# Kernel optimization log

Measured on AMD Instinct MI355X. Metric: run time of the kernel, lower is better.

The kernel has to match this reference:

```python
import jax, jax.numpy as jnp
import numpy as np

TEMPERATURE = 8.0  # sqrt(d_k), d_k = 64

def setup_inputs() -> dict:
    key = jax.random.key(0)
    k1, k2, k3, k4 = jax.random.split(key, 4)
    B, H, S, D = 2, 16, 2048, 64
    q = jax.random.normal(k1, (B, H, S, D), dtype=jnp.float32)
    k = jax.random.normal(k2, (B, H, S, D), dtype=jnp.float32)
    v = jax.random.normal(k3, (B, H, S, D), dtype=jnp.float32)
    # dwm: distance-weight matrix broadcast over heads
    dwm = jax.random.uniform(k4, (B, 1, S, S), dtype=jnp.float32)
    sigma = jnp.ones((1,), dtype=jnp.float32)
    return {"q": q, "k": k, "v": v, "dwm": dwm, "sigma": sigma}

def reference(q, k, v, dwm, sigma):
    # scores: [B,H,S,S]
    attn = jnp.einsum("bhsd,bhtd->bhst", q / TEMPERATURE, k)
    g = jnp.exp(dwm / (sigma ** 2))  # broadcasts [B,1,S,S] -> [B,H,S,S]
    attn = jnp.abs(attn * g)
    attn = jax.nn.softmax(attn, axis=-1)  # dropout is identity in eval
    output = jnp.einsum("bhst,bhtd->bhsd", attn, v)
    return (output, attn)
```

## Files before the change

### kernel.cpp

```cpp
#include <hip/hip_runtime.h>
#include <hip/hip_fp16.h>

#define NB 2
#define NH 16
#define NS 2048
#define ND 64
#define BM 64
#define BN 64
#define KP 72
#define VP 72
#define PP 72

typedef _Float16 half8 __attribute__((ext_vector_type(8)));
typedef float f32x4 __attribute__((ext_vector_type(4)));

__global__ __launch_bounds__(256, 4)
void attn_fused(const float* __restrict__ qg, const float* __restrict__ kgl,
                const float* __restrict__ vgl, const float* __restrict__ dwm,
                const float* __restrict__ sig, float* __restrict__ out0,
                float* __restrict__ attn)
{
    __shared__ _Float16 Khi[BN * KP];
    __shared__ _Float16 Klo[BN * KP];
    __shared__ _Float16 Vs[ND * VP];
    __shared__ _Float16 Ps[BM * PP];

    const int tid  = threadIdx.x;
    const int wave = tid >> 6;
    const int lane = tid & 63;
    const int quad = lane >> 4;
    const int lc   = lane & 15;

    const int mtile = blockIdx.x;
    const int bh    = blockIdx.y;
    const int b     = bh >> 4;

    const float sv = sig[0];
    const float inv_s2 = 1.0f / (sv * sv);

    const float* qp = qg  + (size_t)bh * NS * ND + (size_t)mtile * BM * ND;
    const float* kp = kgl + (size_t)bh * NS * ND;
    const float* vp = vgl + (size_t)bh * NS * ND;
    const float* dp = dwm + (size_t)b  * NS * NS + (size_t)mtile * BM * NS;
    float* op = out0 + (size_t)bh * NS * ND + (size_t)mtile * BM * ND;
    float* ap = attn + (size_t)bh * NS * NS + (size_t)mtile * BM * NS;

    half8 aqh0, aql0, aqh1, aql1;
    {
        const float* qr = qp + (size_t)(wave * 16 + lc) * ND + quad * 8;
        float4 f0 = *(const float4*)qr;
        float4 f1 = *(const float4*)(qr + 4);
        float4 f2 = *(const float4*)(qr + 32);
        float4 f3 = *(const float4*)(qr + 36);
        float v0[8] = {f0.x, f0.y, f0.z, f0.w, f1.x, f1.y, f1.z, f1.w};
        float v1[8] = {f2.x, f2.y, f2.z, f2.w, f3.x, f3.y, f3.z, f3.w};
        #pragma unroll
        for (int j = 0; j < 8; j++) {
            float x = v0[j] * 0.125f;
            _Float16 h = (_Float16)x;
            aqh0[j] = h; aql0[j] = (_Float16)(x - (float)h);
            x = v1[j] * 0.125f;
            h = (_Float16)x;
            aqh1[j] = h; aql1[j] = (_Float16)(x - (float)h);
        }
    }

    auto stageK = [&](int t0) {
        const int r  = tid >> 2;
        const int ds = (tid & 3) * 16;
        const float* s = kp + (size_t)(t0 + r) * ND + ds;
        float4 f0 = *(const float4*)s;
        float4 f1 = *(const float4*)(s + 4);
        float4 f2 = *(const float4*)(s + 8);
        float4 f3 = *(const float4*)(s + 12);
        float fv[16] = {f0.x, f0.y, f0.z, f0.w, f1.x, f1.y, f1.z, f1.w,
                        f2.x, f2.y, f2.z, f2.w, f3.x, f3.y, f3.z, f3.w};
        half8 h0, h1, l0, l1;
        #pragma unroll
        for (int i = 0; i < 8; i++) {
            _Float16 h = (_Float16)fv[i];
            h0[i] = h; l0[i] = (_Float16)(fv[i] - (float)h);
            h = (_Float16)fv[8 + i];
            h1[i] = h; l1[i] = (_Float16)(fv[8 + i] - (float)h);
        }
        *(half8*)&Khi[r * KP + ds]     = h0;
        *(half8*)&Khi[r * KP + ds + 8] = h1;
        *(half8*)&Klo[r * KP + ds]     = l0;
        *(half8*)&Klo[r * KP + ds + 8] = l1;
    };

    auto stageV = [&](int t0) {
        const int tp = tid >> 3;
        const int ds = (tid & 7) * 8;
        const float4* sa = (const float4*)(vp + (size_t)(t0 + 2 * tp) * ND + ds);
        const float4* sb = (const float4*)(vp + (size_t)(t0 + 2 * tp + 1) * ND + ds);
        float4 a0 = sa[0], a1 = sa[1];
        float4 b0 = sb[0], b1 = sb[1];
        float av[8] = {a0.x, a0.y, a0.z, a0.w, a1.x, a1.y, a1.z, a1.w};
        float bv[8] = {b0.x, b0.y, b0.z, b0.w, b1.x, b1.y, b1.z, b1.w};
        unsigned int* Vdw = (unsigned int*)Vs;
        #pragma unroll
        for (int i = 0; i < 8; i++) {
            const int d  = ds + i;
            const int dw = d * (VP / 2) + (tp ^ (((d >> 3) & 7) << 2));
            union { _Float16 h[2]; unsigned int u; } pk;
            pk.h[0] = (_Float16)av[i];
            pk.h[1] = (_Float16)bv[i];
            Vdw[dw] = pk.u;
        }
    };

    float lsum[4] = {0.f, 0.f, 0.f, 0.f};

    for (int t0 = 0; t0 < NS; t0 += BN) {
        __syncthreads();
        stageK(t0);
        __syncthreads();
        #pragma unroll
        for (int n = 0; n < 4; n++) {
            const half8 kh0 = *(const half8*)&Khi[(n * 16 + lc) * KP + quad * 8];
            const half8 kh1 = *(const half8*)&Khi[(n * 16 + lc) * KP + quad * 8 + 32];
            const half8 kl0 = *(const half8*)&Klo[(n * 16 + lc) * KP + quad * 8];
            const half8 kl1 = *(const half8*)&Klo[(n * 16 + lc) * KP + quad * 8 + 32];
            f32x4 c = {0.f, 0.f, 0.f, 0.f};
            c = __builtin_amdgcn_mfma_f32_16x16x32_f16(aqh0, kh0, c, 0, 0, 0);
            c = __builtin_amdgcn_mfma_f32_16x16x32_f16(aqh1, kh1, c, 0, 0, 0);
            c = __builtin_amdgcn_mfma_f32_16x16x32_f16(aql0, kh0, c, 0, 0, 0);
            c = __builtin_amdgcn_mfma_f32_16x16x32_f16(aql1, kh1, c, 0, 0, 0);
            c = __builtin_amdgcn_mfma_f32_16x16x32_f16(aqh0, kl0, c, 0, 0, 0);
            c = __builtin_amdgcn_mfma_f32_16x16x32_f16(aqh1, kl1, c, 0, 0, 0);
            #pragma unroll
            for (int r2 = 0; r2 < 4; r2++) {
                const int lrow = wave * 16 + quad * 4 + r2;
                const int col  = t0 + n * 16 + lc;
                const float g = __expf(dp[(size_t)lrow * NS + col] * inv_s2);
                const float z = fabsf(c[r2] * g);
                lsum[r2] += __expf(z);
            }
        }
    }

    #pragma unroll
    for (int r2 = 0; r2 < 4; r2++) {
        float s = lsum[r2];
        s += __shfl_xor(s, 1, 64);
        s += __shfl_xor(s, 2, 64);
        s += __shfl_xor(s, 4, 64);
        s += __shfl_xor(s, 8, 64);
        lsum[r2] = 1.0f / s;
    }

    f32x4 o[4];
    #pragma unroll
    for (int i = 0; i < 4; i++) o[i] = (f32x4){0.f, 0.f, 0.f, 0.f};

    for (int t0 = 0; t0 < NS; t0 += BN) {
        __syncthreads();
        stageK(t0);
        stageV(t0);
        __syncthreads();
        #pragma unroll
        for (int n = 0; n < 4; n++) {
            const half8 kh0 = *(const half8*)&Khi[(n * 16 + lc) * KP + quad * 8];
            const half8 kh1 = *(const half8*)&Khi[(n * 16 + lc) * KP + quad * 8 + 32];
            const half8 kl0 = *(const half8*)&Klo[(n * 16 + lc) * KP + quad * 8];
            const half8 kl1 = *(const half8*)&Klo[(n * 16 + lc) * KP + quad * 8 + 32];
            f32x4 c = {0.f, 0.f, 0.f, 0.f};
            c = __builtin_amdgcn_mfma_f32_16x16x32_f16(aqh0, kh0, c, 0, 0, 0);
            c = __builtin_amdgcn_mfma_f32_16x16x32_f16(aqh1, kh1, c, 0, 0, 0);
            c = __builtin_amdgcn_mfma_f32_16x16x32_f16(aql0, kh0, c, 0, 0, 0);
            c = __builtin_amdgcn_mfma_f32_16x16x32_f16(aql1, kh1, c, 0, 0, 0);
            c = __builtin_amdgcn_mfma_f32_16x16x32_f16(aqh0, kl0, c, 0, 0, 0);
            c = __builtin_amdgcn_mfma_f32_16x16x32_f16(aqh1, kl1, c, 0, 0, 0);
            #pragma unroll
            for (int r2 = 0; r2 < 4; r2++) {
                const int lrow = wave * 16 + quad * 4 + r2;
                const int col  = t0 + n * 16 + lc;
                const float g = __expf(dp[(size_t)lrow * NS + col] * inv_s2);
                const float z = fabsf(c[r2] * g);
                const float p = __expf(z) * lsum[r2];
                Ps[(size_t)lrow * PP + n * 16 + lc] = (_Float16)p;
            }
        }
        const half8 pa0 = *(const half8*)&Ps[(wave * 16 + lc) * PP + quad * 8];
        const half8 pa1 = *(const half8*)&Ps[(wave * 16 + lc) * PP + quad * 8 + 32];

        {
            float* arow = ap + (size_t)(wave * 16 + lc) * NS + t0 + quad * 8;
            f32x4 s0 = {(float)pa0[0], (float)pa0[1], (float)pa0[2], (float)pa0[3]};
            f32x4 s1 = {(float)pa0[4], (float)pa0[5], (float)pa0[6], (float)pa0[7]};
            f32x4 s2 = {(float)pa1[0], (float)pa1[1], (float)pa1[2], (float)pa1[3]};
            f32x4 s3 = {(float)pa1[4], (float)pa1[5], (float)pa1[6], (float)pa1[7]};
            __builtin_nontemporal_store(s0, (f32x4*)arow);
            __builtin_nontemporal_store(s1, (f32x4*)(arow + 4));
            __builtin_nontemporal_store(s2, (f32x4*)(arow + 32));
            __builtin_nontemporal_store(s3, (f32x4*)(arow + 36));
        }

        #pragma unroll
        for (int n2 = 0; n2 < 4; n2++) {
            const int dv  = n2 * 16 + lc;
            const int fd  = ((dv >> 3) & 7) << 2;
            const int dwb = dv * (VP / 2);
            const half8 bv0 = *(const half8*)((const char*)Vs +
                               (size_t)((dwb + ((quad * 4) ^ fd)) * 4));
            const half8 bv1 = *(const half8*)((const char*)Vs +
                               (size_t)((dwb + ((16 + quad * 4) ^ fd)) * 4));
            o[n2] = __builtin_amdgcn_mfma_f32_16x16x32_f16(pa0, bv0, o[n2], 0, 0, 0);
            o[n2] = __builtin_amdgcn_mfma_f32_16x16x32_f16(pa1, bv1, o[n2], 0, 0, 0);
        }
    }

    #pragma unroll
    for (int n2 = 0; n2 < 4; n2++) {
        #pragma unroll
        for (int r2 = 0; r2 < 4; r2++) {
            const int lrow = wave * 16 + quad * 4 + r2;
            __builtin_nontemporal_store(o[n2][r2],
                                        &op[(size_t)lrow * ND + n2 * 16 + lc]);
        }
    }
}

extern "C" void kernel_launch(void* const* d_in, const int* in_sizes, int n_in,
                              void* d_out, int out_size, void* d_ws, size_t ws_size,
                              hipStream_t stream) {
    (void)in_sizes; (void)n_in; (void)out_size; (void)d_ws; (void)ws_size;
    const float* q   = (const float*)d_in[0];
    const float* k   = (const float*)d_in[1];
    const float* v   = (const float*)d_in[2];
    const float* dwm = (const float*)d_in[3];
    const float* sig = (const float*)d_in[4];
    float* out0 = (float*)d_out;
    float* attn = out0 + (size_t)NB * NH * NS * ND;
    dim3 grid(NS / BM, NB * NH);
    attn_fused<<<grid, dim3(256), 0, stream>>>(q, k, v, dwm, sig, out0, attn);
}
```

Baseline: 810.6 us.

## Pre-convert K/V to swizzled fp16 tiles and stream them via global_load_lds

Adds a prep kernel that splits K into hi/lo fp16 and transposes V into fp16, writing XOR-swizzled tile images to the workspace. The main kernel copies these images straight into LDS with global_load_lds. This removes the per-workgroup fp32 load, conversion and transpose work that was repeated for every query tile. It also remaps workgroup IDs so blocks sharing a head run close together, and raises the occupancy hint to 5 blocks per CU. The costs are an extra kernel launch, a workspace round trip, and a fallback path that only runs when the workspace is too small.

```diff
diff --git a/kernel.cpp b/kernel.cpp
--- a/kernel.cpp
+++ b/kernel.cpp
@@ -7,23 +7,266 @@
 #define ND 64
 #define BM 64
 #define BN 64
+#define NT (NS / BN)
+#define TILE_BYTES 24576
+#define KV_BYTES ((size_t)NB * NH * NT * TILE_BYTES)
+
+#define SW(r) ((((r) & 7) ^ (((r) & 8) >> 2)) << 4)
+
+typedef _Float16 half8 __attribute__((ext_vector_type(8)));
+typedef _Float16 half4 __attribute__((ext_vector_type(4)));
+typedef float f32x4 __attribute__((ext_vector_type(4)));
+
+#define GLDS16(gp, lp) __builtin_amdgcn_global_load_lds(                      \
+    (const __attribute__((address_space(1))) void*)(gp),                      \
+    (__attribute__((address_space(3))) void*)(lp), 16, 0, 0)
+
+__global__ __launch_bounds__(256)
+void prep_kv(const float* __restrict__ kg, const float* __restrict__ vg,
+             char* __restrict__ ws)
+{
+    __shared__ _Float16 T[64][72];
+    const int tile = blockIdx.x, bh = blockIdx.y, tid = threadIdx.x;
+    const float* kp = kg + ((size_t)bh * NS + (size_t)tile * BN) * ND;
+    const float* vp = vg + ((size_t)bh * NS + (size_t)tile * BN) * ND;
+    char* img = ws + ((size_t)(bh * NT + tile)) * TILE_BYTES;
+
+    #pragma unroll
+    for (int i = 0; i < 2; ++i) {
+        const int c = tid + i * 256;
+        const int r = c >> 3, s = c & 7;
+        const float* src = kp + r * ND + s * 8;
+        float4 f0 = *(const float4*)src;
+        float4 f1 = *(const float4*)(src + 4);
+        float fv[8] = {f0.x, f0.y, f0.z, f0.w, f1.x, f1.y, f1.z, f1.w};
+        half8 h, l;
+        #pragma unroll
+        for (int j = 0; j < 8; ++j) {
+            _Float16 hh = (_Float16)fv[j];
+            h[j] = hh; l[j] = (_Float16)(fv[j] - (float)hh);
+        }
+        const int off = r * 128 + ((s << 4) ^ SW(r));
+        *(half8*)(img + off) = h;
+        *(half8*)(img + 8192 + off) = l;
+    }
+    #pragma unroll
+    for (int i = 0; i < 2; ++i) {
+        const int c = tid + i * 256;
+        const int t = c >> 3, ds = (c & 7) * 8;
+        const float* src = vp + t * ND + ds;
+        float4 f0 = *(const float4*)src;
+        float4 f1 = *(const float4*)(src + 4);
+        float fv[8] = {f0.x, f0.y, f0.z, f0.w, f1.x, f1.y, f1.z, f1.w};
+        #pragma unroll
+        for (int j = 0; j < 8; ++j) T[t][ds + j] = (_Float16)fv[j];
+    }
+    __syncthreads();
+    #pragma unroll
+    for (int i = 0; i < 2; ++i) {
+        const int c = tid + i * 256;
+        const int d = c >> 3, s = c & 7;
+        half8 h;
+        #pragma unroll
+        for (int j = 0; j < 8; ++j) h[j] = T[s * 8 + j][d];
+        *(half8*)(img + 16384 + d * 128 + ((s << 4) ^ SW(d))) = h;
+    }
+}
+
+__global__ __launch_bounds__(256, 5)
+void attn_fused(const float* __restrict__ qg, const char* __restrict__ kvws,
+                const float* __restrict__ dwm, const float* __restrict__ sig,
+                float* __restrict__ out0, float* __restrict__ attn)
+{
+    __shared__ char lds[32768];
+    char* const Khi = lds;
+    char* const Klo = lds + 8192;
+    char* const Vs  = lds + 16384;
+    char* const Ps  = lds + 24576;
+
+    const int tid  = threadIdx.x;
+    const int wave = tid >> 6;
+    const int lane = tid & 63;
+    const int quad = lane >> 4;
+    const int lc   = lane & 15;
+
+    const int wg      = blockIdx.x;
+    const int logical = (wg & 7) * 128 + (wg >> 3);
+    const int mtile   = logical & 31;
+    const int bh      = logical >> 5;
+    const int b       = bh >> 4;
+
+    const float sv = sig[0];
+    const float inv_s2 = 1.0f / (sv * sv);
+
+    const float* qp  = qg  + (size_t)bh * NS * ND + (size_t)mtile * BM * ND;
+    const char*  kvb = kvws + (size_t)bh * NT * TILE_BYTES;
+    const float* dp  = dwm + (size_t)b  * NS * NS + (size_t)mtile * BM * NS;
+    float* op = out0 + (size_t)bh * NS * ND + (size_t)mtile * BM * ND;
+    float* ap = attn + (size_t)bh * NS * NS + (size_t)mtile * BM * NS;
+
+    half8 aqh0, aql0, aqh1, aql1;
+    {
+        const float* qr = qp + (size_t)(wave * 16 + lc) * ND + quad * 8;
+        float4 f0 = *(const float4*)qr;
+        float4 f1 = *(const float4*)(qr + 4);
+        float4 f2 = *(const float4*)(qr + 32);
+        float4 f3 = *(const float4*)(qr + 36);
+        float v0[8] = {f0.x, f0.y, f0.z, f0.w, f1.x, f1.y, f1.z, f1.w};
+        float v1[8] = {f2.x, f2.y, f2.z, f2.w, f3.x, f3.y, f3.z, f3.w};
+        #pragma unroll
+        for (int j = 0; j < 8; j++) {
+            float x = v0[j] * 0.125f;
+            _Float16 h = (_Float16)x;
+            aqh0[j] = h; aql0[j] = (_Float16)(x - (float)h);
+            x = v1[j] * 0.125f;
+            h = (_Float16)x;
+            aqh1[j] = h; aql1[j] = (_Float16)(x - (float)h);
+        }
+    }
+
+    float lsum[4] = {0.f, 0.f, 0.f, 0.f};
+
+    for (int t = 0; t < NT; ++t) {
+        const char* img = kvb + (size_t)t * TILE_BYTES;
+        __syncthreads();
+        GLDS16(img +         tid * 16, Khi +        tid * 16);
+        GLDS16(img +  4096 + tid * 16, Khi + 4096 + tid * 16);
+        GLDS16(img +  8192 + tid * 16, Klo +        tid * 16);
+        GLDS16(img + 12288 + tid * 16, Klo + 4096 + tid * 16);
+        __syncthreads();
+        #pragma unroll
+        for (int n = 0; n < 4; ++n) {
+            const int rowK = n * 16 + lc;
+            const int sw = SW(rowK);
+            const char* kb = Khi + rowK * 128;
+            const char* lb = Klo + rowK * 128;
+            const half8 kh0 = *(const half8*)(kb + ((quad * 16) ^ sw));
+            const half8 kh1 = *(const half8*)(kb + ((64 + quad * 16) ^ sw));
+            const half8 kl0 = *(const half8*)(lb + ((quad * 16) ^ sw));
+            const half8 kl1 = *(const half8*)(lb + ((64 + quad * 16) ^ sw));
+            f32x4 c = {0.f, 0.f, 0.f, 0.f};
+            c = __builtin_amdgcn_mfma_f32_16x16x32_f16(aqh0, kh0, c, 0, 0, 0);
+            c = __builtin_amdgcn_mfma_f32_16x16x32_f16(aqh1, kh1, c, 0, 0, 0);
+            c = __builtin_amdgcn_mfma_f32_16x16x32_f16(aql0, kh0, c, 0, 0, 0);
+            c = __builtin_amdgcn_mfma_f32_16x16x32_f16(aql1, kh1, c, 0, 0, 0);
+            c = __builtin_amdgcn_mfma_f32_16x16x32_f16(aqh0, kl0, c, 0, 0, 0);
+            c = __builtin_amdgcn_mfma_f32_16x16x32_f16(aqh1, kl1, c, 0, 0, 0);
+            #pragma unroll
+            for (int r2 = 0; r2 < 4; ++r2) {
+                const int lrow = wave * 16 + quad * 4 + r2;
+                const int col  = t * BN + n * 16 + lc;
+                const float g = __expf(dp[(size_t)lrow * NS + col] * inv_s2);
+                lsum[r2] += __expf(fabsf(c[r2]) * g);
+            }
+        }
+    }
+
+    #pragma unroll
+    for (int r2 = 0; r2 < 4; ++r2) {
+        float s = lsum[r2];
+        s += __shfl_xor(s, 1, 64);
+        s += __shfl_xor(s, 2, 64);
+        s += __shfl_xor(s, 4, 64);
+        s += __shfl_xor(s, 8, 64);
+        lsum[r2] = 1.0f / s;
+    }
+
+    f32x4 o[4];
+    #pragma unroll
+    for (int i = 0; i < 4; i++) o[i] = (f32x4){0.f, 0.f, 0.f, 0.f};
+
+    for (int t = 0; t < NT; ++t) {
+        const char* img = kvb + (size_t)t * TILE_BYTES;
+        __syncthreads();
+        GLDS16(img +         tid * 16, Khi +        tid * 16);
+        GLDS16(img +  4096 + tid * 16, Khi + 4096 + tid * 16);
+        GLDS16(img +  8192 + tid * 16, Klo +        tid * 16);
+        GLDS16(img + 12288 + tid * 16, Klo + 4096 + tid * 16);
+        GLDS16(img + 16384 + tid * 16, Vs  +        tid * 16);
+        GLDS16(img + 20480 + tid * 16, Vs  + 4096 + tid * 16);
+        __syncthreads();
+        #pragma unroll
+        for (int n = 0; n < 4; ++n) {
+            const int rowK = n * 16 + lc;
+            const int sw = SW(rowK);
+            const char* kb = Khi + rowK * 128;
+            const char* lb = Klo + rowK * 128;
+            const half8 kh0 = *(const half8*)(kb + ((quad * 16) ^ sw));
+            const half8 kh1 = *(const half8*)(kb + ((64 + quad * 16) ^ sw));
+            const half8 kl0 = *(const half8*)(lb + ((quad * 16) ^ sw));
+            const half8 kl1 = *(const half8*)(lb + ((64 + quad * 16) ^ sw));
+            f32x4 c = {0.f, 0.f, 0.f, 0.f};
+            c = __builtin_amdgcn_mfma_f32_16x16x32_f16(aqh0, kh0, c, 0, 0, 0);
+            c = __builtin_amdgcn_mfma_f32_16x16x32_f16(aqh1, kh1, c, 0, 0, 0);
+            c = __builtin_amdgcn_mfma_f32_16x16x32_f16(aql0, kh0, c, 0, 0, 0);
+            c = __builtin_amdgcn_mfma_f32_16x16x32_f16(aql1, kh1, c, 0, 0, 0);
+            c = __builtin_amdgcn_mfma_f32_16x16x32_f16(aqh0, kl0, c, 0, 0, 0);
+            c = __builtin_amdgcn_mfma_f32_16x16x32_f16(aqh1, kl1, c, 0, 0, 0);
+            #pragma unroll
+            for (int r2 = 0; r2 < 4; ++r2) {
+                const int lrow = wave * 16 + quad * 4 + r2;
+                const int col  = t * BN + n * 16 + lc;
+                const float g = __expf(dp[(size_t)lrow * NS + col] * inv_s2);
+                const float p = __expf(fabsf(c[r2]) * g) * lsum[r2];
+                *(_Float16*)(Ps + lrow * 128 +
+                             (((n * 16 + lc) * 2) ^ SW(lrow))) = (_Float16)p;
+            }
+        }
+        const int rowP = wave * 16 + lc;
+        const int swp = SW(rowP);
+        const half8 pa0 = *(const half8*)(Ps + rowP * 128 + ((quad * 16) ^ swp));
+        const half8 pa1 = *(const half8*)(Ps + rowP * 128 + ((64 + quad * 16) ^ swp));
+
+        {
+            const int cl = lane & 15, rh = lane >> 4;
+            #pragma unroll
+            for (int g2 = 0; g2 < 4; ++g2) {
+                const int row = wave * 16 + g2 * 4 + rh;
+                const half4 ph = *(const half4*)(Ps + row * 128 +
+                                                 ((cl * 8) ^ SW(row)));
+                f32x4 s = {(float)ph[0], (float)ph[1], (float)ph[2], (float)ph[3]};
+                __builtin_nontemporal_store(
+                    s, (f32x4*)(ap + (size_t)row * NS + t * BN + cl * 4));
+            }
+        }
+
+        #pragma unroll
+        for (int n2 = 0; n2 < 4; ++n2) {
+            const int dv = n2 * 16 + lc;
+            const int swv = SW(dv);
+            const char* vb = Vs + dv * 128;
+            const half8 bv0 = *(const half8*)(vb + ((quad * 16) ^ swv));
+            const half8 bv1 = *(const half8*)(vb + ((64 + quad * 16) ^ swv));
+            o[n2] = __builtin_amdgcn_mfma_f32_16x16x32_f16(pa0, bv0, o[n2], 0, 0, 0);
+            o[n2] = __builtin_amdgcn_mfma_f32_16x16x32_f16(pa1, bv1, o[n2], 0, 0, 0);
+        }
+    }
+
+    #pragma unroll
+    for (int n2 = 0; n2 < 4; ++n2) {
+        #pragma unroll
+        for (int r2 = 0; r2 < 4; ++r2) {
+            const int lrow = wave * 16 + quad * 4 + r2;
+            __builtin_nontemporal_store(o[n2][r2],
+                                        &op[(size_t)lrow * ND + n2 * 16 + lc]);
+        }
+    }
+}
+
 #define KP 72
 #define VP 72
 #define PP 72
 
-typedef _Float16 half8 __attribute__((ext_vector_type(8)));
-typedef float f32x4 __attribute__((ext_vector_type(4)));
-
 __global__ __launch_bounds__(256, 4)
-void attn_fused(const float* __restrict__ qg, const float* __restrict__ kgl,
-                const float* __restrict__ vgl, const float* __restrict__ dwm,
-                const float* __restrict__ sig, float* __restrict__ out0,
-                float* __restrict__ attn)
+void attn_fused_legacy(const float* __restrict__ qg, const float* __restrict__ kgl,
+                       const float* __restrict__ vgl, const float* __restrict__ dwm,
+                       const float* __restrict__ sig, float* __restrict__ out0,
+                       float* __restrict__ attn)
 {
     __shared__ _Float16 Khi[BN * KP];
     __shared__ _Float16 Klo[BN * KP];
-    __shared__ _Float16 Vs[ND * VP];
-    __shared__ _Float16 Ps[BM * PP];
+    __shared__ _Float16 Vsl[ND * VP];
+    __shared__ _Float16 Psl[BM * PP];
 
     const int tid  = threadIdx.x;
     const int wave = tid >> 6;
@@ -98,7 +341,7 @@
         float4 b0 = sb[0], b1 = sb[1];
         float av[8] = {a0.x, a0.y, a0.z, a0.w, a1.x, a1.y, a1.z, a1.w};
         float bv[8] = {b0.x, b0.y, b0.z, b0.w, b1.x, b1.y, b1.z, b1.w};
-        unsigned int* Vdw = (unsigned int*)Vs;
+        unsigned int* Vdw = (unsigned int*)Vsl;
         #pragma unroll
         for (int i = 0; i < 8; i++) {
             const int d  = ds + i;
@@ -179,11 +422,11 @@
                 const float g = __expf(dp[(size_t)lrow * NS + col] * inv_s2);
                 const float z = fabsf(c[r2] * g);
                 const float p = __expf(z) * lsum[r2];
-                Ps[(size_t)lrow * PP + n * 16 + lc] = (_Float16)p;
+                Psl[(size_t)lrow * PP + n * 16 + lc] = (_Float16)p;
             }
         }
-        const half8 pa0 = *(const half8*)&Ps[(wave * 16 + lc) * PP + quad * 8];
-        const half8 pa1 = *(const half8*)&Ps[(wave * 16 + lc) * PP + quad * 8 + 32];
+        const half8 pa0 = *(const half8*)&Psl[(wave * 16 + lc) * PP + quad * 8];
+        const half8 pa1 = *(const half8*)&Psl[(wave * 16 + lc) * PP + quad * 8 + 32];
 
         {
             float* arow = ap + (size_t)(wave * 16 + lc) * NS + t0 + quad * 8;
@@ -202,9 +445,9 @@
             const int dv  = n2 * 16 + lc;
             const int fd  = ((dv >> 3) & 7) << 2;
             const int dwb = dv * (VP / 2);
-            const half8 bv0 = *(const half8*)((const char*)Vs +
+            const half8 bv0 = *(const half8*)((const char*)Vsl +
                                (size_t)((dwb + ((quad * 4) ^ fd)) * 4));
-            const half8 bv1 = *(const half8*)((const char*)Vs +
+            const half8 bv1 = *(const half8*)((const char*)Vsl +
                                (size_t)((dwb + ((16 + quad * 4) ^ fd)) * 4));
             o[n2] = __builtin_amdgcn_mfma_f32_16x16x32_f16(pa0, bv0, o[n2], 0, 0, 0);
             o[n2] = __builtin_amdgcn_mfma_f32_16x16x32_f16(pa1, bv1, o[n2], 0, 0, 0);
@@ -225,7 +468,7 @@
 extern "C" void kernel_launch(void* const* d_in, const int* in_sizes, int n_in,
                               void* d_out, int out_size, void* d_ws, size_t ws_size,
                               hipStream_t stream) {
-    (void)in_sizes; (void)n_in; (void)out_size; (void)d_ws; (void)ws_size;
+    (void)in_sizes; (void)n_in; (void)out_size;
     const float* q   = (const float*)d_in[0];
     const float* k   = (const float*)d_in[1];
     const float* v   = (const float*)d_in[2];
@@ -233,6 +476,15 @@
     const float* sig = (const float*)d_in[4];
     float* out0 = (float*)d_out;
     float* attn = out0 + (size_t)NB * NH * NS * ND;
-    dim3 grid(NS / BM, NB * NH);
-    attn_fused<<<grid, dim3(256), 0, stream>>>(q, k, v, dwm, sig, out0, attn);
+
+    if (d_ws != nullptr && ws_size >= KV_BYTES) {
+        char* ws = (char*)d_ws;
+        prep_kv<<<dim3(NT, NB * NH), dim3(256), 0, stream>>>(k, v, ws);
+        attn_fused<<<dim3(NT * NB * NH), dim3(256), 0, stream>>>(
+            q, ws, dwm, sig, out0, attn);
+    } else {
+        dim3 grid(NS / BM, NB * NH);
+        attn_fused_legacy<<<grid, dim3(256), 0, stream>>>(
+            q, k, v, dwm, sig, out0, attn);
+    }
 }
```

Result: slower. 883.8 us (+9.0%).
